# Performance work log

Measured on AMD Instinct MI355X. Metric: run time of the kernel, lower is better.

Reference implementation:

```python
import jax, jax.numpy as jnp
import numpy as np

MODEL = 1024
HEADS = 16
HEAD_DIM = MODEL // HEADS
INNER = 4096
EPS = 1e-5


def _layer_norm(x, gamma, beta):
    mu = jnp.mean(x, axis=-1, keepdims=True)
    var = jnp.mean((x - mu) ** 2, axis=-1, keepdims=True)
    return (x - mu) * jax.lax.rsqrt(var + EPS) * gamma + beta


def setup_inputs() -> dict:
    key = jax.random.key(0)
    ks = jax.random.split(key, 12)
    B, S = 4, 2048
    s_in = 1.0 / np.sqrt(MODEL)
    s_ff = 1.0 / np.sqrt(INNER)
    return {
        "x": jax.random.normal(ks[0], (B, S, MODEL), jnp.float32),
        "mask": jnp.ones((B, 1, 1, S), jnp.int32),
        "Wq": jax.random.normal(ks[1], (MODEL, MODEL), jnp.float32) * s_in,
        "bq": jnp.zeros((MODEL,), jnp.float32),
        "Wk": jax.random.normal(ks[2], (MODEL, MODEL), jnp.float32) * s_in,
        "bk": jnp.zeros((MODEL,), jnp.float32),
        "Wv": jax.random.normal(ks[3], (MODEL, MODEL), jnp.float32) * s_in,
        "bv": jnp.zeros((MODEL,), jnp.float32),
        "Wo": jax.random.normal(ks[4], (MODEL, MODEL), jnp.float32) * s_in,
        "bo": jnp.zeros((MODEL,), jnp.float32),
        "g1": jnp.ones((MODEL,), jnp.float32),
        "beta1": jnp.zeros((MODEL,), jnp.float32),
        "W1": jax.random.normal(ks[5], (MODEL, INNER), jnp.float32) * s_in,
        "b1": jnp.zeros((INNER,), jnp.float32),
        "W2": jax.random.normal(ks[6], (INNER, MODEL), jnp.float32) * s_ff,
        "b2": jnp.zeros((MODEL,), jnp.float32),
        "g2": jnp.ones((MODEL,), jnp.float32),
        "beta2": jnp.zeros((MODEL,), jnp.float32),
    }


def reference(x, mask, Wq, bq, Wk, bk, Wv, bv, Wo, bo, g1, beta1, W1, b1, W2, b2, g2, beta2):
    B, S, _ = x.shape
    temp = jnp.sqrt(jnp.float32(HEAD_DIM))
    # projections -> [B, H, S, Dh]
    q = (x @ Wq + bq).reshape(B, S, HEADS, HEAD_DIM).transpose(0, 2, 1, 3)
    k = (x @ Wk + bk).reshape(B, S, HEADS, HEAD_DIM).transpose(0, 2, 1, 3)
    v = (x @ Wv + bv).reshape(B, S, HEADS, HEAD_DIM).transpose(0, 2, 1, 3)
    # scores [B, H, S, S]
    scores = jnp.einsum("bhqd,bhkd->bhqk", q / temp, k)
    scores = jnp.where(mask == 0, jnp.float32(-1e10), scores)
    attn = jax.nn.softmax(scores, axis=-1)
    ctx = jnp.einsum("bhqk,bhkd->bhqd", attn, v)
    ctx = ctx.transpose(0, 2, 1, 3).reshape(B, S, MODEL)
    attn_out = ctx @ Wo + bo
    x = _layer_norm(x + attn_out, g1, beta1)
    ff = jax.nn.relu(x @ W1 + b1) @ W2 + b2
    x = _layer_norm(x + ff, g2, beta2)
    return x
```

## Files before the change

### kernel.cpp

```cpp
#include <hip/hip_runtime.h>
#include <stdint.h>

#define MODEL 1024
#define INNER 4096
#define NHEADS 16
#define HDIM 64
#define BATCH 4
#define SEQ 2048
#define MROWS (BATCH*SEQ)

typedef __bf16 bf16x8 __attribute__((ext_vector_type(8)));
typedef float f32x4 __attribute__((ext_vector_type(4)));
typedef unsigned short ushort4v __attribute__((ext_vector_type(4)));

__device__ __forceinline__ unsigned short f2bf(float f) {
  unsigned u = __builtin_bit_cast(unsigned, f);
  u += 0x7FFFu + ((u >> 16) & 1u);
  return (unsigned short)(u >> 16);
}
__device__ __forceinline__ unsigned packbf_trunc(float lo, float hi) {
  return (__builtin_bit_cast(unsigned, hi) & 0xFFFF0000u) |
         (__builtin_bit_cast(unsigned, lo) >> 16);
}

#define AS1 __attribute__((address_space(1)))
#define AS3 __attribute__((address_space(3)))
__device__ __forceinline__ void gload_lds16(const void* g, void* l) {
  __builtin_amdgcn_global_load_lds((const AS1 void*)g, (AS3 void*)l, 16, 0, 0);
}

__global__ __launch_bounds__(256) void k_cvt(const float* __restrict__ in,
                                             unsigned short* __restrict__ out, int n4) {
  int i = blockIdx.x * 256 + threadIdx.x;
  if (i < n4) {
    float4 v = ((const float4*)in)[i];
    ushort4v o = { f2bf(v.x), f2bf(v.y), f2bf(v.z), f2bf(v.w) };
    ((ushort4v*)out)[i] = o;
  }
}

__global__ __launch_bounds__(256) void k_bcat(const float* __restrict__ bq,
                                              const float* __restrict__ bk,
                                              const float* __restrict__ bv,
                                              float* __restrict__ o) {
  int i = blockIdx.x * 256 + threadIdx.x;
  o[i] = (i < 1024) ? bq[i] : (i < 2048) ? bk[i - 1024] : bv[i - 2048];
}

__global__ __launch_bounds__(256) void k_transpose(const float* __restrict__ W,
                                                   unsigned short* __restrict__ Wt,
                                                   int K, int N) {
  __shared__ float tile[32][33];
  const int n0 = blockIdx.x * 32, k0 = blockIdx.y * 32;
  const int c = threadIdx.x & 31, r4 = threadIdx.x >> 5;
#pragma unroll
  for (int i = 0; i < 4; i++) {
    int r = r4 + i * 8;
    tile[r][c] = W[(size_t)(k0 + r) * N + n0 + c];
  }
  __syncthreads();
#pragma unroll
  for (int i = 0; i < 4; i++) {
    int r = r4 + i * 8;
    Wt[(size_t)(n0 + r) * K + k0 + c] = f2bf(tile[c][r]);
  }
}

template <int MODE, bool SPLIT>
__global__ __launch_bounds__(512, 2) void k_gemm(const unsigned short* __restrict__ A,
                                                 const unsigned short* __restrict__ Bt,
                                                 const float* __restrict__ bias,
                                                 void* __restrict__ out0,
                                                 void* __restrict__ out1,
                                                 void* __restrict__ out2,
                                                 int M, int N, int Kfull) {
  __shared__ unsigned short As[3 * 256 * 32];
  __shared__ unsigned short Bs[3 * 256 * 32];
  const int t = threadIdx.x;
  const int lane = t & 63;
  const int w = t >> 6;
  const int li = lane & 15, lg = lane >> 4;
  const int wm8 = w >> 2, wn4 = w & 3;

  const unsigned nwg = gridDim.x * gridDim.y;
  const unsigned lin = blockIdx.y * gridDim.x + blockIdx.x;
  const unsigned q8 = nwg >> 3, r8 = nwg & 7, xcd = lin & 7, pos = lin >> 3;
  const unsigned swz = (xcd < r8 ? xcd * (q8 + 1) : r8 * (q8 + 1) + (xcd - r8) * q8) + pos;
  int bx = swz % gridDim.x, by = swz / gridDim.x;

  int kp = 0, Ksub = Kfull;
  if (SPLIT) {
    const int hx = gridDim.x >> 1;
    kp = bx >= hx;
    bx -= kp * hx;
    Ksub = Kfull >> 1;
  }
  const int bm = by * 256, bn = bx * 256;
  const size_t koff = (size_t)kp * Ksub;
  const int NT = Ksub / 32;

  const int sr0 = w * 16 + (lane >> 2);
  const int sr1 = sr0 + 128;
  const int sl = lane & 3;
  const unsigned short* pA0 = A + (size_t)(bm + sr0) * Kfull + koff + ((sl ^ ((sr0 >> 1) & 3)) << 3);
  const unsigned short* pA1 = A + (size_t)(bm + sr1) * Kfull + koff + ((sl ^ ((sr1 >> 1) & 3)) << 3);
  const unsigned short* pB0 = Bt + (size_t)(bn + sr0) * Kfull + koff + ((sl ^ ((sr0 >> 1) & 3)) << 3);
  const unsigned short* pB1 = Bt + (size_t)(bn + sr1) * Kfull + koff + ((sl ^ ((sr1 >> 1) & 3)) << 3);

  f32x4 acc[8][4] = {};

  auto stageA = [&](int buf, int tt) {
    gload_lds16(pA0 + tt * 32, &As[buf * 8192 + w * 512]);
    gload_lds16(pA1 + tt * 32, &As[buf * 8192 + 4096 + w * 512]);
  };
  auto stageB = [&](int buf, int tt) {
    gload_lds16(pB0 + tt * 32, &Bs[buf * 8192 + w * 512]);
    gload_lds16(pB1 + tt * 32, &Bs[buf * 8192 + 4096 + w * 512]);
  };

  stageA(0, 0); stageB(0, 0);
  stageA(1, 1); stageB(1, 1);
  asm volatile("s_waitcnt vmcnt(4)" ::: "memory");
  __builtin_amdgcn_s_barrier();

  int buf = 0;
  for (int tt = 0; tt < NT; ++tt) {
    const int nb = (buf + 2 >= 3) ? buf - 1 : buf + 2;
    const unsigned short* Ab = &As[buf * 8192];
    const unsigned short* Bb = &Bs[buf * 8192];
    bf16x8 av[4], bv_[4];
#pragma unroll
    for (int m = 0; m < 4; m++) {
      const int r = wm8 * 128 + m * 16 + li;
      av[m] = *(const bf16x8*)&Ab[r * 32 + ((lg ^ ((r >> 1) & 3)) << 3)];
    }
#pragma unroll
    for (int n = 0; n < 4; n++) {
      const int r = wn4 * 64 + n * 16 + li;
      bv_[n] = *(const bf16x8*)&Bb[r * 32 + ((lg ^ ((r >> 1) & 3)) << 3)];
    }
    if (tt + 2 < NT) stageA(nb, tt + 2);
    __builtin_amdgcn_s_barrier();
    __builtin_amdgcn_s_setprio(1);
#pragma unroll
    for (int m = 0; m < 4; m++)
#pragma unroll
      for (int n = 0; n < 4; n++)
        acc[m][n] = __builtin_amdgcn_mfma_f32_16x16x32_bf16(av[m], bv_[n], acc[m][n], 0, 0, 0);
    __builtin_amdgcn_s_setprio(0);
    bf16x8 av2[4];
#pragma unroll
    for (int m = 0; m < 4; m++) {
      const int r = wm8 * 128 + 64 + m * 16 + li;
      av2[m] = *(const bf16x8*)&Ab[r * 32 + ((lg ^ ((r >> 1) & 3)) << 3)];
    }
    if (tt + 2 < NT) stageB(nb, tt + 2);
    __builtin_amdgcn_s_barrier();
    __builtin_amdgcn_s_setprio(1);
#pragma unroll
    for (int m = 0; m < 4; m++)
#pragma unroll
      for (int n = 0; n < 4; n++)
        acc[m + 4][n] = __builtin_amdgcn_mfma_f32_16x16x32_bf16(av2[m], bv_[n], acc[m + 4][n], 0, 0, 0);
    __builtin_amdgcn_s_setprio(0);
    if (tt + 2 < NT) asm volatile("s_waitcnt vmcnt(4)" ::: "memory");
    else             asm volatile("s_waitcnt vmcnt(0)" ::: "memory");
    __builtin_amdgcn_s_barrier();
    buf = (buf == 2) ? 0 : buf + 1;
  }

#pragma unroll
  for (int m = 0; m < 8; m++) {
    const int row0 = bm + wm8 * 128 + m * 16 + lg * 4;
#pragma unroll
    for (int n = 0; n < 4; n++) {
      const int gcol = bn + wn4 * 64 + n * 16 + li;
      if (MODE == 0) {
        float* dst = (float*)(kp ? out1 : out0);
        const float bvc = (!SPLIT || kp == 0) ? bias[gcol] : 0.f;
#pragma unroll
        for (int j = 0; j < 4; j++)
          dst[(size_t)(row0 + j) * N + gcol] = acc[m][n][j] + bvc;
      } else if (MODE == 2) {
        const float bvc = bias[gcol];
#pragma unroll
        for (int j = 0; j < 4; j++)
          ((unsigned short*)out0)[(size_t)(row0 + j) * N + gcol] = f2bf(fmaxf(acc[m][n][j] + bvc, 0.f));
      } else {
        const float bvc = bias[gcol];
        const int region = gcol >> 10, lcol = gcol & 1023;
        if (region < 2) {
          unsigned short* dst = (unsigned short*)(region ? out1 : out0);
#pragma unroll
          for (int j = 0; j < 4; j++)
            dst[(size_t)(row0 + j) * MODEL + lcol] = f2bf(acc[m][n][j] + bvc);
        } else {
          ushort4v o = {f2bf(acc[m][n][0] + bvc), f2bf(acc[m][n][1] + bvc),
                        f2bf(acc[m][n][2] + bvc), f2bf(acc[m][n][3] + bvc)};
          *(ushort4v*)&((unsigned short*)out2)[(size_t)lcol * MROWS + row0] = o;
        }
      }
    }
  }
}

__global__ __launch_bounds__(256, 3) void k_attn(const unsigned short* __restrict__ q,
                                                 const unsigned short* __restrict__ kptr,
                                                 const unsigned short* __restrict__ vt,
                                                 const int* __restrict__ mask,
                                                 unsigned short* __restrict__ ctx) {
  __shared__ unsigned short Ks[2][64 * 64];
  __shared__ unsigned short Vs[2][64 * 64];
  __shared__ unsigned short Ps[4][32 * 64];
  const int t = threadIdx.x, lane = t & 63, w = t >> 6;
  const int li = lane & 15, lg = lane >> 4;
  const int bh = blockIdx.y, b = bh >> 4, h = bh & 15;
  const int q0 = blockIdx.x * 128;
  const size_t basebs = (size_t)b * SEQ;
  const int sw = 8 * (li & 7);
  const int srow = lane >> 3;
  const int scsw = ((lane & 7) ^ srow) * 8;

  auto stageKV = [&](int buf, int kt) {
#pragma unroll
    for (int i = 0; i < 2; i++) {
      const int row = i * 32 + w * 8 + srow;
      gload_lds16(kptr + (basebs + kt + row) * MODEL + h * 64 + scsw,
                  &Ks[buf][i * 2048 + w * 512]);
    }
#pragma unroll
    for (int i = 0; i < 2; i++) {
      const int row = i * 32 + w * 8 + srow;
      gload_lds16(vt + (size_t)(h * 64 + row) * MROWS + basebs + kt + scsw,
                  &Vs[buf][i * 2048 + w * 512]);
    }
  };

  stageKV(0, 0);

  bf16x8 qf[2][2];
#pragma unroll
  for (int m = 0; m < 2; m++)
#pragma unroll
    for (int kk = 0; kk < 2; kk++) {
      int row = q0 + w * 32 + m * 16 + li;
      qf[m][kk] = *(const bf16x8*)&q[(basebs + row) * MODEL + h * 64 + kk * 32 + lg * 8];
    }

  f32x4 acc_oT[4][2] = {};
  float mrow[2] = {-3e38f, -3e38f}, lrow[2] = {0.f, 0.f};

  int cur = 0;
  for (int kt = 0; kt < SEQ; kt += 64) {
    int4 mk4[4];
#pragma unroll
    for (int n = 0; n < 4; n++)
      mk4[n] = *(const int4*)&mask[b * SEQ + kt + n * 16 + lg * 4];

    const bool notlast = (kt + 64 < SEQ);
    if (notlast) {
      stageKV(cur ^ 1, kt + 64);
      asm volatile("s_waitcnt vmcnt(8)" ::: "memory");
    } else {
      asm volatile("s_waitcnt vmcnt(4)" ::: "memory");
    }
    __builtin_amdgcn_s_barrier();

    f32x4 sacc[2][4] = {};
#pragma unroll
    for (int n = 0; n < 4; n++) {
      const int rb = (n * 16 + li) * 64;
      bf16x8 kf0 = *(const bf16x8*)&Ks[cur][rb + ((lg * 8) ^ sw)];
      bf16x8 kf1 = *(const bf16x8*)&Ks[cur][rb + ((32 + lg * 8) ^ sw)];
#pragma unroll
      for (int m = 0; m < 2; m++) {
        sacc[m][n] = __builtin_amdgcn_mfma_f32_16x16x32_bf16(kf0, qf[m][0], sacc[m][n], 0, 0, 0);
        sacc[m][n] = __builtin_amdgcn_mfma_f32_16x16x32_bf16(kf1, qf[m][1], sacc[m][n], 0, 0, 0);
      }
    }

    int mand = mk4[0].x & mk4[0].y & mk4[0].z & mk4[0].w;
    mand &= mk4[1].x & mk4[1].y & mk4[1].z & mk4[1].w;
    mand &= mk4[2].x & mk4[2].y & mk4[2].z & mk4[2].w;
    mand &= mk4[3].x & mk4[3].y & mk4[3].z & mk4[3].w;
    const bool fast = __all(mand != 0);

#pragma unroll
    for (int m = 0; m < 2; m++) {
      float rmax = -3e38f;
      if (fast) {
#pragma unroll
        for (int n = 0; n < 4; n++)
#pragma unroll
          for (int j = 0; j < 4; j++) {
            float sv = sacc[m][n][j] * 0.125f;
            sacc[m][n][j] = sv;
            rmax = fmaxf(rmax, sv);
          }
      } else {
#pragma unroll
        for (int n = 0; n < 4; n++) {
          const int mks[4] = {mk4[n].x, mk4[n].y, mk4[n].z, mk4[n].w};
#pragma unroll
          for (int j = 0; j < 4; j++) {
            float sv = sacc[m][n][j] * 0.125f;
            sv = (mks[j] == 0) ? -1e10f : sv;
            sacc[m][n][j] = sv;
            rmax = fmaxf(rmax, sv);
          }
        }
      }
      rmax = fmaxf(rmax, __shfl_xor(rmax, 16));
      rmax = fmaxf(rmax, __shfl_xor(rmax, 32));
      if (!__all(rmax <= mrow[m] + 8.f)) {
        float mnew = fmaxf(mrow[m], rmax);
        float alpha = __expf(mrow[m] - mnew);
        mrow[m] = mnew;
        lrow[m] *= alpha;
#pragma unroll
        for (int nd = 0; nd < 4; nd++)
#pragma unroll
          for (int j = 0; j < 4; j++) acc_oT[nd][m][j] *= alpha;
      }
      float rsum = 0.f;
#pragma unroll
      for (int n = 0; n < 4; n++)
#pragma unroll
        for (int j = 0; j < 4; j++) {
          float pv = __expf(sacc[m][n][j] - mrow[m]);
          sacc[m][n][j] = pv;
          rsum += pv;
        }
      rsum += __shfl_xor(rsum, 16);
      rsum += __shfl_xor(rsum, 32);
      lrow[m] += rsum;
#pragma unroll
      for (int n = 0; n < 4; n++) {
        uint2 pk = {packbf_trunc(sacc[m][n][0], sacc[m][n][1]),
                    packbf_trunc(sacc[m][n][2], sacc[m][n][3])};
        *(uint2*)&Ps[w][(m * 16 + li) * 64 + ((n * 16 + lg * 4) ^ sw)] = pk;
      }
    }
    asm volatile("s_waitcnt lgkmcnt(0)" ::: "memory");

#pragma unroll
    for (int n2 = 0; n2 < 2; n2++) {
      const int kof = (n2 * 32 + lg * 8) ^ sw;
      bf16x8 pa0 = *(const bf16x8*)&Ps[w][li * 64 + kof];
      bf16x8 pa1 = *(const bf16x8*)&Ps[w][(16 + li) * 64 + kof];
#pragma unroll
      for (int nd = 0; nd < 4; nd++) {
        bf16x8 vfr = *(const bf16x8*)&Vs[cur][(nd * 16 + li) * 64 + kof];
        acc_oT[nd][0] = __builtin_amdgcn_mfma_f32_16x16x32_bf16(vfr, pa0, acc_oT[nd][0], 0, 0, 0);
        acc_oT[nd][1] = __builtin_amdgcn_mfma_f32_16x16x32_bf16(vfr, pa1, acc_oT[nd][1], 0, 0, 0);
      }
    }
    __builtin_amdgcn_sched_barrier(0);
    __builtin_amdgcn_s_barrier();
    cur ^= 1;
  }

#pragma unroll
  for (int m = 0; m < 2; m++) {
    const float rl = 1.f / lrow[m];
    const size_t rowoff = (basebs + q0 + w * 32 + m * 16 + li) * (size_t)MODEL + h * 64;
#pragma unroll
    for (int nd = 0; nd < 4; nd++) {
      ushort4v o = {f2bf(acc_oT[nd][m][0] * rl), f2bf(acc_oT[nd][m][1] * rl),
                    f2bf(acc_oT[nd][m][2] * rl), f2bf(acc_oT[nd][m][3] * rl)};
      *(ushort4v*)&ctx[rowoff + nd * 16 + lg * 4] = o;
    }
  }
}

template <bool WB>
__global__ __launch_bounds__(256) void k_ln3(const float* __restrict__ a,
                                             const float* __restrict__ b0,
                                             const float* __restrict__ b1,
                                             const float* __restrict__ gamma,
                                             const float* __restrict__ beta,
                                             float* __restrict__ outf,
                                             unsigned short* __restrict__ outb) {
  const int row = blockIdx.x;
  const int t = threadIdx.x;
  const size_t off = (size_t)row * MODEL + t * 4;
  float4 xa = *(const float4*)&a[off];
  float4 x0 = *(const float4*)&b0[off];
  float4 x1 = *(const float4*)&b1[off];
  float z0 = xa.x + x0.x + x1.x, z1 = xa.y + x0.y + x1.y;
  float z2 = xa.z + x0.z + x1.z, z3 = xa.w + x0.w + x1.w;
  float s = z0 + z1 + z2 + z3;
  float ss = z0 * z0 + z1 * z1 + z2 * z2 + z3 * z3;
#pragma unroll
  for (int o = 1; o < 64; o <<= 1) { s += __shfl_xor(s, o); ss += __shfl_xor(ss, o); }
  __shared__ float red[8];
  const int lane = t & 63, w = t >> 6;
  if (lane == 0) { red[w] = s; red[4 + w] = ss; }
  __syncthreads();
  s = red[0] + red[1] + red[2] + red[3];
  ss = red[4] + red[5] + red[6] + red[7];
  float mu = s * (1.f / MODEL);
  float var = ss * (1.f / MODEL) - mu * mu;
  float inv = rsqrtf(var + 1e-5f);
  float4 g = *(const float4*)&gamma[t * 4];
  float4 be = *(const float4*)&beta[t * 4];
  float o0 = (z0 - mu) * inv * g.x + be.x;
  float o1 = (z1 - mu) * inv * g.y + be.y;
  float o2 = (z2 - mu) * inv * g.z + be.z;
  float o3 = (z3 - mu) * inv * g.w + be.w;
  float4 ov = {o0, o1, o2, o3};
  *(float4*)&outf[off] = ov;
  if (WB) {
    ushort4v ob = {f2bf(o0), f2bf(o1), f2bf(o2), f2bf(o3)};
    *(ushort4v*)&outb[off] = ob;
  }
}

extern "C" void kernel_launch(void* const* d_in, const int* in_sizes, int n_in,
                              void* d_out, int out_size, void* d_ws, size_t ws_size,
                              hipStream_t stream) {
  (void)in_sizes; (void)n_in; (void)out_size; (void)ws_size;
  const float* x   = (const float*)d_in[0];
  const int*   mask= (const int*)d_in[1];
  const float* Wq  = (const float*)d_in[2];
  const float* bq  = (const float*)d_in[3];
  const float* Wk  = (const float*)d_in[4];
  const float* bk  = (const float*)d_in[5];
  const float* Wv  = (const float*)d_in[6];
  const float* bv  = (const float*)d_in[7];
  const float* Wo  = (const float*)d_in[8];
  const float* bo  = (const float*)d_in[9];
  const float* g1  = (const float*)d_in[10];
  const float* be1 = (const float*)d_in[11];
  const float* W1  = (const float*)d_in[12];
  const float* b1  = (const float*)d_in[13];
  const float* W2  = (const float*)d_in[14];
  const float* b2  = (const float*)d_in[15];
  const float* g2  = (const float*)d_in[16];
  const float* be2 = (const float*)d_in[17];
  float* out = (float*)d_out;

  char* p = (char*)d_ws;
  auto alloc = [&](size_t bytes) { char* r = p; p += (bytes + 255) & ~(size_t)255; return r; };
  unsigned short* xb    = (unsigned short*)alloc((size_t)MROWS * MODEL * 2);
  unsigned short* y1b   = (unsigned short*)alloc((size_t)MROWS * MODEL * 2);
  unsigned short* WqkvT = (unsigned short*)alloc((size_t)3 * MODEL * MODEL * 2);
  unsigned short* WoT   = (unsigned short*)alloc((size_t)MODEL * MODEL * 2);
  unsigned short* W1T   = (unsigned short*)alloc((size_t)MODEL * INNER * 2);
  unsigned short* W2T   = (unsigned short*)alloc((size_t)INNER * MODEL * 2);
  float* bqkv           = (float*)alloc(3072 * 4);
  unsigned short* qb    = (unsigned short*)alloc((size_t)MROWS * MODEL * 2);
  unsigned short* kb    = (unsigned short*)alloc((size_t)MROWS * MODEL * 2);
  unsigned short* vtb   = (unsigned short*)alloc((size_t)MODEL * MROWS * 2);
  unsigned short* ctxb  = (unsigned short*)alloc((size_t)MROWS * MODEL * 2);
  float* attn_out       = (float*)alloc((size_t)MROWS * MODEL * 4);
  float* y1f            = (float*)alloc((size_t)MROWS * MODEL * 4);
  unsigned short* h1 = qb;
  float* p1wo = (float*)kb;
  float* ff   = attn_out;
  float* p1ff = (float*)xb;

  k_cvt<<<(MROWS * MODEL / 4) / 256, 256, 0, stream>>>(x, xb, MROWS * MODEL / 4);
  k_bcat<<<12, 256, 0, stream>>>(bq, bk, bv, bqkv);
  k_transpose<<<dim3(MODEL / 32, MODEL / 32), 256, 0, stream>>>(Wq, WqkvT, MODEL, MODEL);
  k_transpose<<<dim3(MODEL / 32, MODEL / 32), 256, 0, stream>>>(Wk, WqkvT + (size_t)MODEL * MODEL, MODEL, MODEL);
  k_transpose<<<dim3(MODEL / 32, MODEL / 32), 256, 0, stream>>>(Wv, WqkvT + (size_t)2 * MODEL * MODEL, MODEL, MODEL);
  k_transpose<<<dim3(MODEL / 32, MODEL / 32), 256, 0, stream>>>(Wo, WoT, MODEL, MODEL);
  k_transpose<<<dim3(INNER / 32, MODEL / 32), 256, 0, stream>>>(W1, W1T, MODEL, INNER);
  k_transpose<<<dim3(MODEL / 32, INNER / 32), 256, 0, stream>>>(W2, W2T, INNER, MODEL);

  k_gemm<3, false><<<dim3(12, MROWS / 256), 512, 0, stream>>>(xb, WqkvT, bqkv, qb, kb, vtb, MROWS, 3072, MODEL);

  k_attn<<<dim3(SEQ / 128, BATCH * NHEADS), 256, 0, stream>>>(qb, kb, vtb, mask, ctxb);

  k_gemm<0, true><<<dim3(8, MROWS / 256), 512, 0, stream>>>(ctxb, WoT, bo, attn_out, p1wo, nullptr, MROWS, MODEL, MODEL);

  k_ln3<true><<<MROWS, 256, 0, stream>>>(x, attn_out, p1wo, g1, be1, y1f, y1b);

  k_gemm<2, false><<<dim3(INNER / 256, MROWS / 256), 512, 0, stream>>>(y1b, W1T, b1, h1, nullptr, nullptr, MROWS, INNER, MODEL);

  k_gemm<0, true><<<dim3(8, MROWS / 256), 512, 0, stream>>>(h1, W2T, b2, ff, p1ff, nullptr, MROWS, MODEL, INNER);

  k_ln3<false><<<MROWS, 256, 0, stream>>>(y1f, ff, p1ff, g2, be2, out, nullptr);
}
```

Before: 465.7 us.

## Fold softmax scale into Q, use exp2, compute row sums via MFMA

The QKV GEMM epilogue now pre-multiplies Q by 0.125*log2(e), so the attention kernel drops the per-score scale multiply and can use native exp2. The row sum of probabilities moves from VALU adds and cross-lane shuffles to an extra MFMA against a ones vector, which sums the bf16-rounded P that is actually used for P·V. The lazy-rescale threshold is widened to match the log2 domain, and s_setprio brackets the MFMA sections to favour matrix issue across waves. The extra MFMAs add matrix-core work, and native exp2 lowers exp precision.

```diff
diff --git a/kernel.cpp b/kernel.cpp
--- a/kernel.cpp
+++ b/kernel.cpp
@@ -9,9 +9,14 @@
 #define SEQ 2048
 #define MROWS (BATCH*SEQ)
 
+#define QSCALE 0.18033688011112042f
+#define DEFER_THR 11.541560327111708f
+
 typedef __bf16 bf16x8 __attribute__((ext_vector_type(8)));
 typedef float f32x4 __attribute__((ext_vector_type(4)));
 typedef unsigned short ushort4v __attribute__((ext_vector_type(4)));
+
+extern "C" __device__ float __ocml_native_exp2_f32(float);
 
 __device__ __forceinline__ unsigned short f2bf(float f) {
   unsigned u = __builtin_bit_cast(unsigned, f);
@@ -191,9 +196,10 @@
         const int region = gcol >> 10, lcol = gcol & 1023;
         if (region < 2) {
           unsigned short* dst = (unsigned short*)(region ? out1 : out0);
+          const float sc = region ? 1.f : QSCALE;
 #pragma unroll
           for (int j = 0; j < 4; j++)
-            dst[(size_t)(row0 + j) * MODEL + lcol] = f2bf(acc[m][n][j] + bvc);
+            dst[(size_t)(row0 + j) * MODEL + lcol] = f2bf((acc[m][n][j] + bvc) * sc);
         } else {
           ushort4v o = {f2bf(acc[m][n][0] + bvc), f2bf(acc[m][n][1] + bvc),
                         f2bf(acc[m][n][2] + bvc), f2bf(acc[m][n][3] + bvc)};
@@ -247,8 +253,13 @@
       qf[m][kk] = *(const bf16x8*)&q[(basebs + row) * MODEL + h * 64 + kk * 32 + lg * 8];
     }
 
+  const unsigned short one_bits = 0x3F80;
+  const __bf16 oneb = __builtin_bit_cast(__bf16, one_bits);
+  const bf16x8 ones = {oneb, oneb, oneb, oneb, oneb, oneb, oneb, oneb};
+
   f32x4 acc_oT[4][2] = {};
-  float mrow[2] = {-3e38f, -3e38f}, lrow[2] = {0.f, 0.f};
+  f32x4 acc_l[2] = {};
+  float mrow[2] = {-3e38f, -3e38f};
 
   int cur = 0;
   for (int kt = 0; kt < SEQ; kt += 64) {
@@ -267,6 +278,7 @@
     __builtin_amdgcn_s_barrier();
 
     f32x4 sacc[2][4] = {};
+    __builtin_amdgcn_s_setprio(1);
 #pragma unroll
     for (int n = 0; n < 4; n++) {
       const int rb = (n * 16 + li) * 64;
@@ -278,6 +290,7 @@
         sacc[m][n] = __builtin_amdgcn_mfma_f32_16x16x32_bf16(kf1, qf[m][1], sacc[m][n], 0, 0, 0);
       }
     }
+    __builtin_amdgcn_s_setprio(0);
 
     int mand = mk4[0].x & mk4[0].y & mk4[0].z & mk4[0].w;
     mand &= mk4[1].x & mk4[1].y & mk4[1].z & mk4[1].w;
@@ -287,62 +300,45 @@
 
 #pragma unroll
     for (int m = 0; m < 2; m++) {
-      float rmax = -3e38f;
-      if (fast) {
-#pragma unroll
-        for (int n = 0; n < 4; n++)
-#pragma unroll
-          for (int j = 0; j < 4; j++) {
-            float sv = sacc[m][n][j] * 0.125f;
-            sacc[m][n][j] = sv;
-            rmax = fmaxf(rmax, sv);
-          }
-      } else {
+      if (!fast) {
 #pragma unroll
         for (int n = 0; n < 4; n++) {
           const int mks[4] = {mk4[n].x, mk4[n].y, mk4[n].z, mk4[n].w};
 #pragma unroll
-          for (int j = 0; j < 4; j++) {
-            float sv = sacc[m][n][j] * 0.125f;
-            sv = (mks[j] == 0) ? -1e10f : sv;
-            sacc[m][n][j] = sv;
-            rmax = fmaxf(rmax, sv);
-          }
+          for (int j = 0; j < 4; j++)
+            sacc[m][n][j] = (mks[j] == 0) ? -1e30f : sacc[m][n][j];
         }
       }
+      float t0 = fmaxf(fmaxf(sacc[m][0][0], sacc[m][0][1]), fmaxf(sacc[m][0][2], sacc[m][0][3]));
+      float t1 = fmaxf(fmaxf(sacc[m][1][0], sacc[m][1][1]), fmaxf(sacc[m][1][2], sacc[m][1][3]));
+      float t2 = fmaxf(fmaxf(sacc[m][2][0], sacc[m][2][1]), fmaxf(sacc[m][2][2], sacc[m][2][3]));
+      float t3 = fmaxf(fmaxf(sacc[m][3][0], sacc[m][3][1]), fmaxf(sacc[m][3][2], sacc[m][3][3]));
+      float rmax = fmaxf(fmaxf(t0, t1), fmaxf(t2, t3));
       rmax = fmaxf(rmax, __shfl_xor(rmax, 16));
       rmax = fmaxf(rmax, __shfl_xor(rmax, 32));
-      if (!__all(rmax <= mrow[m] + 8.f)) {
+      if (!__all(rmax <= mrow[m] + DEFER_THR)) {
         float mnew = fmaxf(mrow[m], rmax);
-        float alpha = __expf(mrow[m] - mnew);
+        float alpha = __ocml_native_exp2_f32(mrow[m] - mnew);
         mrow[m] = mnew;
-        lrow[m] *= alpha;
+        acc_l[m] *= alpha;
 #pragma unroll
         for (int nd = 0; nd < 4; nd++)
 #pragma unroll
           for (int j = 0; j < 4; j++) acc_oT[nd][m][j] *= alpha;
       }
-      float rsum = 0.f;
-#pragma unroll
-      for (int n = 0; n < 4; n++)
-#pragma unroll
-        for (int j = 0; j < 4; j++) {
-          float pv = __expf(sacc[m][n][j] - mrow[m]);
-          sacc[m][n][j] = pv;
-          rsum += pv;
-        }
-      rsum += __shfl_xor(rsum, 16);
-      rsum += __shfl_xor(rsum, 32);
-      lrow[m] += rsum;
 #pragma unroll
       for (int n = 0; n < 4; n++) {
-        uint2 pk = {packbf_trunc(sacc[m][n][0], sacc[m][n][1]),
-                    packbf_trunc(sacc[m][n][2], sacc[m][n][3])};
+        float p0 = __ocml_native_exp2_f32(sacc[m][n][0] - mrow[m]);
+        float p1 = __ocml_native_exp2_f32(sacc[m][n][1] - mrow[m]);
+        float p2 = __ocml_native_exp2_f32(sacc[m][n][2] - mrow[m]);
+        float p3 = __ocml_native_exp2_f32(sacc[m][n][3] - mrow[m]);
+        uint2 pk = {packbf_trunc(p0, p1), packbf_trunc(p2, p3)};
         *(uint2*)&Ps[w][(m * 16 + li) * 64 + ((n * 16 + lg * 4) ^ sw)] = pk;
       }
     }
     asm volatile("s_waitcnt lgkmcnt(0)" ::: "memory");
 
+    __builtin_amdgcn_s_setprio(1);
 #pragma unroll
     for (int n2 = 0; n2 < 2; n2++) {
       const int kof = (n2 * 32 + lg * 8) ^ sw;
@@ -354,7 +350,10 @@
         acc_oT[nd][0] = __builtin_amdgcn_mfma_f32_16x16x32_bf16(vfr, pa0, acc_oT[nd][0], 0, 0, 0);
         acc_oT[nd][1] = __builtin_amdgcn_mfma_f32_16x16x32_bf16(vfr, pa1, acc_oT[nd][1], 0, 0, 0);
       }
-    }
+      acc_l[0] = __builtin_amdgcn_mfma_f32_16x16x32_bf16(ones, pa0, acc_l[0], 0, 0, 0);
+      acc_l[1] = __builtin_amdgcn_mfma_f32_16x16x32_bf16(ones, pa1, acc_l[1], 0, 0, 0);
+    }
+    __builtin_amdgcn_s_setprio(0);
     __builtin_amdgcn_sched_barrier(0);
     __builtin_amdgcn_s_barrier();
     cur ^= 1;
@@ -362,7 +361,7 @@
 
 #pragma unroll
   for (int m = 0; m < 2; m++) {
-    const float rl = 1.f / lrow[m];
+    const float rl = 1.f / acc_l[m][0];
     const size_t rowoff = (basebs + q0 + w * 32 + m * 16 + li) * (size_t)MODEL + h * 64;
 #pragma unroll
     for (int nd = 0; nd < 4; nd++) {
```

New measurement: 457.2 us. No clear change (-1.8%).
